# Performance work log

Measured on AMD Instinct MI355X. Metric: run time of the kernel, lower is better.

## Reference

```python
import jax, jax.numpy as jnp
import numpy as np

B = 8192   # batch / node count
D = 1024   # feature dim
K = 20     # k nearest neighbors (k+1 = 21 edges per row incl. self)


def setup_inputs() -> dict:
    key = jax.random.key(0)
    k1, k2 = jax.random.split(key)
    x = jax.random.normal(k1, (B, D), dtype=jnp.float32)
    # nn.init.normal_(edge_weights, mean=1.0, std=0.01)
    edge_weights = 1.0 + 0.01 * jax.random.normal(k2, (K + 1,), dtype=jnp.float32)
    return {"x": x, "edge_weights": edge_weights}


def reference(x, edge_weights):
    # F.normalize(x, p=2, dim=1): divide by max(||x||, eps)
    norm = jnp.maximum(jnp.linalg.norm(x, axis=1, keepdims=True), 1e-12)
    xn = x / norm
    adj = xn @ xn.T                                  # [B, B] cosine similarity
    _, idx = jax.lax.top_k(adj, K + 1)               # [B, K+1] neighbor indices
    rows = jnp.arange(B)[:, None]                    # [B, 1]
    # scatter learned per-rank edge weights; topk indices are distinct per row,
    # so set() matches the torch per-rank assignment loop (mask is redundant).
    w = jnp.zeros((B, B), dtype=x.dtype).at[rows, idx].set(
        jnp.broadcast_to(edge_weights, (B, K + 1))
    )
    row_sum = w.sum(axis=1, keepdims=True) + 1e-8
    return w / row_sum
```

## Files before the change

kernel.cpp:

```cpp
#include <hip/hip_runtime.h>
#include <hip/hip_bf16.h>
#include <float.h>
#include <math.h>

#define B_N 8192
#define D_N 1024
#define KP1 21
#define THRESH0 0.07f
#define MARGIN 1.5e-3f
#define CAND_CAP 64
#define SURV_CAP 256

typedef __attribute__((ext_vector_type(8))) short short8;
typedef __attribute__((ext_vector_type(4))) float floatx4;

__device__ __forceinline__ unsigned short f32_to_bf16_rtne(float f) {
    unsigned int u = __float_as_uint(f);
    unsigned int r = (u + 0x7FFFu + ((u >> 16) & 1u)) >> 16;
    return (unsigned short)r;
}

__device__ __forceinline__ void async_copy16(const void* g, void* l) {
    __builtin_amdgcn_global_load_lds(
        (const __attribute__((address_space(1))) void*)g,
        (__attribute__((address_space(3))) void*)l, 16, 0, 0);
}

__global__ __launch_bounds__(256) void normalize_kernel(const float* __restrict__ x,
                                                        float* __restrict__ xn32,
                                                        unsigned short* __restrict__ xbf) {
    int row = blockIdx.x;
    int t = threadIdx.x;
    const float* xr = x + (size_t)row * D_N;
    float v[4];
#pragma unroll
    for (int m = 0; m < 4; ++m) v[m] = xr[t + 256 * m];
    double s = 0.0;
#pragma unroll
    for (int m = 0; m < 4; ++m) { double d = (double)v[m]; s += d * d; }
#pragma unroll
    for (int off = 32; off > 0; off >>= 1) s += __shfl_down(s, off, 64);
    __shared__ double p[4];
    if ((t & 63) == 0) p[t >> 6] = s;
    __syncthreads();
    double nrm = sqrt(p[0] + p[1] + p[2] + p[3]);
    if (nrm < 1e-12) nrm = 1e-12;
    float* xo = xn32 + (size_t)row * D_N;
    unsigned short* xb = xbf + (size_t)row * D_N;
#pragma unroll
    for (int m = 0; m < 4; ++m) {
        float q = (float)((double)v[m] / nrm);
        xo[t + 256 * m] = q;
        xb[t + 256 * m] = f32_to_bf16_rtne(q);
    }
}

__global__ __launch_bounds__(256) void mfma_gemm_kernel(const unsigned short* __restrict__ xb,
                                                        unsigned short* __restrict__ gram) {
    __shared__ unsigned char smem[33280];
    const int bx = blockIdx.x, by = blockIdx.y;
    if (bx < by) return;
    unsigned char* As = smem;
    unsigned char* Bs = smem + 16384;
    const int t = threadIdx.x;
    const int lane = t & 63;
    const int w = t >> 6;
    const int wr = w >> 1, wc = w & 1;
    const char* Ag = (const char*)xb + (size_t)(by * 128) * 2048;
    const char* Bg = (const char*)xb + (size_t)(bx * 128) * 2048;

    int goff[4], loff[4];
#pragma unroll
    for (int q = 0; q < 4; ++q) {
        int e = w * 4 + q;
        int r = e * 8 + (lane >> 3);
        int ch = (lane & 7) ^ (lane >> 3);
        goff[q] = r * 2048 + ch * 16;
        loff[q] = e * 1024;
    }

    int kc = lane >> 4, rl = lane & 15;
    int aoff[2][4], boff[2][4];
#pragma unroll
    for (int s = 0; s < 2; ++s)
#pragma unroll
        for (int i = 0; i < 4; ++i) {
            int a_r = wr * 64 + i * 16 + rl;
            aoff[s][i] = a_r * 128 + (((s * 4 + kc) ^ (rl & 7)) << 4);
            int b_r = wc * 64 + i * 16 + rl;
            boff[s][i] = b_r * 128 + (((s * 4 + kc) ^ (rl & 7)) << 4);
        }

    floatx4 acc[4][4] = {};
    for (int kb = 0; kb < D_N; kb += 64) {
        int koff = kb * 2;
#pragma unroll
        for (int q = 0; q < 4; ++q) async_copy16(Ag + goff[q] + koff, As + loff[q]);
#pragma unroll
        for (int q = 0; q < 4; ++q) async_copy16(Bg + goff[q] + koff, Bs + loff[q]);
        __syncthreads();
#pragma unroll
        for (int s = 0; s < 2; ++s) {
            short8 af[4], bfv[4];
#pragma unroll
            for (int i = 0; i < 4; ++i) af[i] = *(const short8*)(As + aoff[s][i]);
#pragma unroll
            for (int i = 0; i < 4; ++i) bfv[i] = *(const short8*)(Bs + boff[s][i]);
#pragma unroll
            for (int mi = 0; mi < 4; ++mi)
#pragma unroll
                for (int nj = 0; nj < 4; ++nj)
                    acc[mi][nj] = __builtin_amdgcn_mfma_f32_16x16x32_bf16(af[mi], bfv[nj], acc[mi][nj], 0, 0, 0);
        }
        __syncthreads();
    }

    int lrow = wr * 64 + (lane >> 4) * 4;
    int lcol = wc * 64 + (lane & 15);
    unsigned short* tile = (unsigned short*)smem;
#pragma unroll
    for (int mi = 0; mi < 4; ++mi)
#pragma unroll
        for (int nj = 0; nj < 4; ++nj)
#pragma unroll
            for (int e = 0; e < 4; ++e) {
                unsigned short hv = f32_to_bf16_rtne(acc[mi][nj][e]);
                gram[(size_t)(by * 128 + lrow + mi * 16 + e) * B_N + bx * 128 + lcol + nj * 16] = hv;
                tile[(lrow + mi * 16 + e) * 130 + lcol + nj * 16] = hv;
            }
    if (bx != by) {
        __syncthreads();
        int j = t >> 1, h = t & 1;
        unsigned short* orow = gram + (size_t)(bx * 128 + j) * B_N + by * 128 + h * 64;
#pragma unroll
        for (int c = 0; c < 8; ++c) {
            unsigned short v[8];
#pragma unroll
            for (int ii = 0; ii < 8; ++ii)
                v[ii] = tile[(h * 64 + c * 8 + ii) * 130 + j];
            *(uint4*)(orow + c * 8) = *(const uint4*)v;
        }
    }
}

__global__ __launch_bounds__(256) void compact_rescore_out_kernel(const unsigned short* __restrict__ gram,
                                                                  const float* __restrict__ xn32,
                                                                  const float* __restrict__ ew,
                                                                  float* __restrict__ out) {
    __shared__ float4 xi4[D_N / 4];
    __shared__ unsigned int skey[SURV_CAP];
    __shared__ int scol[SURV_CAP];
    __shared__ int hist1[256];
    __shared__ int hist2[256];
    __shared__ int cidx[CAND_CAP];
    __shared__ double ssc[CAND_CAP];
    __shared__ int sid[CAND_CAP];
    __shared__ int widx[KP1];
    __shared__ float wval[KP1];
    __shared__ int scnt, ccnt, key21s;
    int row = blockIdx.x, t = threadIdx.x;
    int lane = t & 63, w = t >> 6;

    xi4[t] = ((const float4*)(xn32 + (size_t)row * D_N))[t];
    hist1[t] = 0;
    if (t < CAND_CAP) { ssc[t] = -DBL_MAX; sid[t] = 0x7FFFFFFF; }
    if (t == 0) { scnt = 0; ccnt = 0; key21s = 0; }
    __syncthreads();

    const uint4* gu4 = (const uint4*)(gram + (size_t)row * B_N);
#pragma unroll
    for (int m = 0; m < 4; ++m) {
        uint4 pr = gu4[t + 256 * m];
        unsigned int w4[4] = {pr.x, pr.y, pr.z, pr.w};
        int base = (t + 256 * m) * 8;
#pragma unroll
        for (int q = 0; q < 4; ++q) {
            unsigned int k0 = w4[q] & 0xFFFFu;
            unsigned int k1 = w4[q] >> 16;
            float v0 = __uint_as_float(k0 << 16);
            float v1 = __uint_as_float(k1 << 16);
            if (v0 > THRESH0) {
                int p = atomicAdd(&scnt, 1);
                if (p < SURV_CAP) { skey[p] = k0; scol[p] = base + q * 2; atomicAdd(&hist1[k0 >> 8], 1); }
            }
            if (v1 > THRESH0) {
                int p = atomicAdd(&scnt, 1);
                if (p < SURV_CAP) { skey[p] = k1; scol[p] = base + q * 2 + 1; atomicAdd(&hist1[k1 >> 8], 1); }
            }
        }
    }
    __syncthreads();
    int sc = scnt < SURV_CAP ? scnt : SURV_CAP;

    if (w == 0) {
        int h0 = hist1[4 * lane], h1 = hist1[4 * lane + 1], h2 = hist1[4 * lane + 2], h3 = hist1[4 * lane + 3];
        int sl = h0 + h1 + h2 + h3;
        int v = sl;
#pragma unroll
        for (int off = 1; off < 64; off <<= 1) {
            int u = __shfl_down(v, off, 64);
            if (lane + off < 64) v += u;
        }
        int E = v - sl;
        int T3 = E, T2 = E + h3, T1 = T2 + h2, Tc0 = T1 + h1;
        int Hl = -1, Rl = 0;
        if      (T3  < KP1 && KP1 <= T3  + h3) { Hl = 4 * lane + 3; Rl = KP1 - T3; }
        else if (T2  < KP1 && KP1 <= T2  + h2) { Hl = 4 * lane + 2; Rl = KP1 - T2; }
        else if (T1  < KP1 && KP1 <= T1  + h1) { Hl = 4 * lane + 1; Rl = KP1 - T1; }
        else if (Tc0 < KP1 && KP1 <= Tc0 + h0) { Hl = 4 * lane;     Rl = KP1 - Tc0; }
        unsigned long long bal = __ballot(Hl >= 0);
        if (bal) {
            int src = __ffsll((long long)bal) - 1;
            int H = __shfl(Hl, src, 64);
            int R = __shfl(Rl, src, 64);
#pragma unroll
            for (int i = 0; i < 4; ++i) hist2[4 * lane + i] = 0;
#pragma unroll
            for (int r = 0; r < 4; ++r) {
                int s = lane + 64 * r;
                if (s < sc) {
                    unsigned int k = skey[s];
                    if ((int)(k >> 8) == H) atomicAdd(&hist2[k & 255], 1);
                }
            }
            int g0 = hist2[4 * lane], g1 = hist2[4 * lane + 1], g2 = hist2[4 * lane + 2], g3 = hist2[4 * lane + 3];
            int sl2 = g0 + g1 + g2 + g3;
            int v2 = sl2;
#pragma unroll
            for (int off = 1; off < 64; off <<= 1) {
                int u = __shfl_down(v2, off, 64);
                if (lane + off < 64) v2 += u;
            }
            int E2 = v2 - sl2;
            int U3 = E2, U2 = E2 + g3, U1 = U2 + g2, Uc0 = U1 + g1;
            int Ll = -1;
            if      (U3  < R && R <= U3  + g3) Ll = 4 * lane + 3;
            else if (U2  < R && R <= U2  + g2) Ll = 4 * lane + 2;
            else if (U1  < R && R <= U1  + g1) Ll = 4 * lane + 1;
            else if (Uc0 < R && R <= Uc0 + g0) Ll = 4 * lane;
            if (Ll >= 0) key21s = (H << 8) | Ll;
        }
    }
    __syncthreads();

    float v21 = __uint_as_float((unsigned int)key21s << 16);
    float cutoff = v21 - MARGIN;
    if (t < sc) {
        float vf = __uint_as_float(skey[t] << 16);
        if (vf >= cutoff) {
            int p = atomicAdd(&ccnt, 1);
            if (p < CAND_CAP) cidx[p] = scol[t];
        }
    }
    __syncthreads();
    int count = ccnt < CAND_CAP ? ccnt : CAND_CAP;

    for (int c = w; c < count; c += 4) {
        int j = cidx[c];
        if (j >= 0 && j < B_N) {
            const float4* xj4 = (const float4*)(xn32 + (size_t)j * D_N);
            double s = 0.0;
#pragma unroll
            for (int m = 0; m < 4; ++m) {
                float4 a = xi4[lane + 64 * m];
                float4 b = xj4[lane + 64 * m];
                s = fma((double)a.x, (double)b.x, s);
                s = fma((double)a.y, (double)b.y, s);
                s = fma((double)a.z, (double)b.z, s);
                s = fma((double)a.w, (double)b.w, s);
            }
#pragma unroll
            for (int off = 32; off > 0; off >>= 1) s += __shfl_down(s, off, 64);
            if (lane == 0) { ssc[c] = s; sid[c] = j; }
        }
    }
    __syncthreads();

    if (w == 0) {
        double mv = ssc[lane];
        int mi = sid[lane];
#pragma unroll
        for (int k = 2; k <= 64; k <<= 1) {
#pragma unroll
            for (int j = 32; j > 0; j >>= 1) {
                if (j < k) {
                    double ov = __shfl_xor(mv, j, 64);
                    int oi = __shfl_xor(mi, j, 64);
                    bool iLower = (lane & j) == 0;
                    bool dirDesc = (lane & k) == 0;
                    bool other_first = (ov > mv) || (ov == mv && oi < mi);
                    bool take = (iLower == dirDesc) ? other_first : !other_first;
                    if (take) { mv = ov; mi = oi; }
                }
            }
        }
        if (lane < KP1) {
            double s = 1e-8;
#pragma unroll
            for (int k = 0; k < KP1; ++k) s += (double)ew[k];
            widx[lane] = mi;
            wval[lane] = (float)((double)ew[lane] / s);
        }
    }
    __syncthreads();

    float* orow = out + (size_t)row * B_N;
    float4* orow4 = (float4*)orow;
    float4 z = make_float4(0.f, 0.f, 0.f, 0.f);
#pragma unroll
    for (int m = 0; m < 8; ++m) orow4[t + 256 * m] = z;
    __syncthreads();
    if (t < KP1) {
        int c = widx[t];
        if (c >= 0 && c < B_N) orow[c] = wval[t];
    }
}

extern "C" void kernel_launch(void* const* d_in, const int* in_sizes, int n_in,
                              void* d_out, int out_size, void* d_ws, size_t ws_size,
                              hipStream_t stream) {
    const float* x = (const float*)d_in[0];
    const float* ew = (const float*)d_in[1];

    unsigned short* gram = (unsigned short*)d_ws;
    float* xn32 = (float*)((char*)d_ws + ((size_t)128 << 20));
    unsigned short* xbf = (unsigned short*)((char*)d_ws + ((size_t)160 << 20));

    normalize_kernel<<<B_N, 256, 0, stream>>>(x, xn32, xbf);
    mfma_gemm_kernel<<<dim3(B_N / 128, B_N / 128), 256, 0, stream>>>(xbf, gram);
    compact_rescore_out_kernel<<<B_N, 256, 0, stream>>>(gram, xn32, ew, (float*)d_out);
}
```

Measured before the change: 517.7 us.

## Use triangular 1D grid and tiled gram layout with coalesced tile stores

Launches only the upper-triangular 2080 GEMM tiles via a closed-form index-to-(by,bx) mapping instead of a full 64x64 grid with early exits. Stores the bf16 Gram matrix in a 128x128 tile-contiguous layout, written as coalesced 16-byte vectors staged through LDS, with a rotated read pattern for the transposed tile to reduce bank conflicts. The rescore kernel's row reads are re-indexed to match the tiled layout, so each row read now touches 64 separate 256-byte segments rather than one contiguous row.

```diff
diff --git a/kernel.cpp b/kernel.cpp
--- a/kernel.cpp
+++ b/kernel.cpp
@@ -58,8 +58,12 @@
 __global__ __launch_bounds__(256) void mfma_gemm_kernel(const unsigned short* __restrict__ xb,
                                                         unsigned short* __restrict__ gram) {
     __shared__ unsigned char smem[33280];
-    const int bx = blockIdx.x, by = blockIdx.y;
-    if (bx < by) return;
+    int i = blockIdx.x;
+    int by = (int)((129.0f - sqrtf(16641.0f - 8.0f * (float)i)) * 0.5f);
+    while (by > 0 && by * (129 - by) / 2 > i) --by;
+    while ((by + 1) * (128 - by) / 2 <= i) ++by;
+    int bx = by + (i - by * (129 - by) / 2);
+
     unsigned char* As = smem;
     unsigned char* Bs = smem + 16384;
     const int t = threadIdx.x;
@@ -84,11 +88,11 @@
 #pragma unroll
     for (int s = 0; s < 2; ++s)
 #pragma unroll
-        for (int i = 0; i < 4; ++i) {
-            int a_r = wr * 64 + i * 16 + rl;
-            aoff[s][i] = a_r * 128 + (((s * 4 + kc) ^ (rl & 7)) << 4);
-            int b_r = wc * 64 + i * 16 + rl;
-            boff[s][i] = b_r * 128 + (((s * 4 + kc) ^ (rl & 7)) << 4);
+        for (int ii = 0; ii < 4; ++ii) {
+            int a_r = wr * 64 + ii * 16 + rl;
+            aoff[s][ii] = a_r * 128 + (((s * 4 + kc) ^ (rl & 7)) << 4);
+            int b_r = wc * 64 + ii * 16 + rl;
+            boff[s][ii] = b_r * 128 + (((s * 4 + kc) ^ (rl & 7)) << 4);
         }
 
     floatx4 acc[4][4] = {};
@@ -103,9 +107,9 @@
         for (int s = 0; s < 2; ++s) {
             short8 af[4], bfv[4];
 #pragma unroll
-            for (int i = 0; i < 4; ++i) af[i] = *(const short8*)(As + aoff[s][i]);
-#pragma unroll
-            for (int i = 0; i < 4; ++i) bfv[i] = *(const short8*)(Bs + boff[s][i]);
+            for (int ii = 0; ii < 4; ++ii) af[ii] = *(const short8*)(As + aoff[s][ii]);
+#pragma unroll
+            for (int ii = 0; ii < 4; ++ii) bfv[ii] = *(const short8*)(Bs + boff[s][ii]);
 #pragma unroll
             for (int mi = 0; mi < 4; ++mi)
 #pragma unroll
@@ -123,22 +127,33 @@
 #pragma unroll
         for (int nj = 0; nj < 4; ++nj)
 #pragma unroll
-            for (int e = 0; e < 4; ++e) {
-                unsigned short hv = f32_to_bf16_rtne(acc[mi][nj][e]);
-                gram[(size_t)(by * 128 + lrow + mi * 16 + e) * B_N + bx * 128 + lcol + nj * 16] = hv;
-                tile[(lrow + mi * 16 + e) * 130 + lcol + nj * 16] = hv;
-            }
+            for (int e = 0; e < 4; ++e)
+                tile[(lrow + mi * 16 + e) * 130 + lcol + nj * 16] = f32_to_bf16_rtne(acc[mi][nj][e]);
+    __syncthreads();
+
+    int rt = t >> 4;
+    int cb = (t & 15) * 8;
+    uint4* ntile = (uint4*)(gram + ((size_t)(by * 64 + bx) << 14));
+#pragma unroll
+    for (int c = 0; c < 8; ++c) {
+        int r = c * 16 + rt;
+        unsigned short v[8];
+#pragma unroll
+        for (int ii = 0; ii < 8; ++ii) v[ii] = tile[r * 130 + cb + ii];
+        ntile[c * 256 + t] = *(const uint4*)v;
+    }
     if (bx != by) {
-        __syncthreads();
-        int j = t >> 1, h = t & 1;
-        unsigned short* orow = gram + (size_t)(bx * 128 + j) * B_N + by * 128 + h * 64;
+        uint4* ttile = (uint4*)(gram + ((size_t)(bx * 64 + by) << 14));
 #pragma unroll
         for (int c = 0; c < 8; ++c) {
+            int r = c * 16 + rt;
             unsigned short v[8];
 #pragma unroll
-            for (int ii = 0; ii < 8; ++ii)
-                v[ii] = tile[(h * 64 + c * 8 + ii) * 130 + j];
-            *(uint4*)(orow + c * 8) = *(const uint4*)v;
+            for (int s = 0; s < 8; ++s) {
+                int ii = (s + (lane >> 2)) & 7;
+                v[ii] = tile[(cb + ii) * 130 + r];
+            }
+            ttile[c * 256 + t] = *(const uint4*)v;
         }
     }
 }
@@ -167,12 +182,13 @@
     if (t == 0) { scnt = 0; ccnt = 0; key21s = 0; }
     __syncthreads();
 
-    const uint4* gu4 = (const uint4*)(gram + (size_t)row * B_N);
+    const uint4* grow = (const uint4*)gram + (size_t)(row >> 7) * 64 * 2048 + (size_t)(row & 127) * 16;
 #pragma unroll
     for (int m = 0; m < 4; ++m) {
-        uint4 pr = gu4[t + 256 * m];
+        int g = t + 256 * m;
+        uint4 pr = grow[(size_t)(g >> 4) * 2048 + (g & 15)];
         unsigned int w4[4] = {pr.x, pr.y, pr.z, pr.w};
-        int base = (t + 256 * m) * 8;
+        int base = ((g >> 4) << 7) + ((g & 15) << 3);
 #pragma unroll
         for (int q = 0; q < 4; ++q) {
             unsigned int k0 = w4[q] & 0xFFFFu;
@@ -214,7 +230,7 @@
             int H = __shfl(Hl, src, 64);
             int R = __shfl(Rl, src, 64);
 #pragma unroll
-            for (int i = 0; i < 4; ++i) hist2[4 * lane + i] = 0;
+            for (int ii = 0; ii < 4; ++ii) hist2[4 * lane + ii] = 0;
 #pragma unroll
             for (int r = 0; r < 4; ++r) {
                 int s = lane + 64 * r;
@@ -327,6 +343,6 @@
     unsigned short* xbf = (unsigned short*)((char*)d_ws + ((size_t)160 << 20));
 
     normalize_kernel<<<B_N, 256, 0, stream>>>(x, xn32, xbf);
-    mfma_gemm_kernel<<<dim3(B_N / 128, B_N / 128), 256, 0, stream>>>(xbf, gram);
+    mfma_gemm_kernel<<<2080, 256, 0, stream>>>(xbf, gram);
     compact_rescore_out_kernel<<<B_N, 256, 0, stream>>>(gram, xn32, ew, (float*)d_out);
 }
```

After: 508.4 us. No clear change (-1.8%).
